# Performance work log

Hardware: AMD Instinct MI355X
Metric: run time of the kernel (lower is better)

## Reference

```python
import jax, jax.numpy as jnp
import numpy as np

B, N, M, C, H, D = 1, 4096, 4096, 768, 12, 64  # batch, tgt len, src len, in_dim, heads, head_dim
SCALE = D ** -0.5


def setup_inputs() -> dict:
    key = jax.random.key(0)
    ks = jax.random.split(key, 6)
    s = 0.02
    return {
        "x": jax.random.normal(ks[0], (B, N, C), jnp.float32),
        "src": jax.random.normal(ks[1], (B, M, C), jnp.float32),
        "W_qv": jax.random.normal(ks[2], (2 * H * D, C), jnp.float32) * s,
        "W_k": jax.random.normal(ks[3], (H * D, C), jnp.float32) * s,
        "W_proj": jax.random.normal(ks[4], (C, H * D), jnp.float32) * s,
        "b_proj": jnp.zeros((C,), jnp.float32),
    }


def reference(x, src, W_qv, W_k, W_proj, b_proj):
    Bb, Nn, _ = x.shape
    Mm = src.shape[1]
    # q, v come from src; k comes from x (info flows src -> target)
    qv = (src @ W_qv.T).reshape(Bb, Mm, 2, H, D)
    q = qv[:, :, 0].transpose(0, 2, 1, 3)  # (B, H, M, D)
    v = qv[:, :, 1].transpose(0, 2, 1, 3)  # (B, H, M, D)
    k = (x @ W_k.T).reshape(Bb, Nn, H, D) * SCALE  # (B, N, H, D), pre-scaled
    # attn[b,h,n,m] = q[b,h,m,:] . k[b,n,h,:]  (torch: (q @ k).transpose(-2,-1))
    attn = jnp.einsum('bhmd,bnhd->bhnm', q, k)
    attn = jax.nn.softmax(attn, axis=-1)  # softmax over src tokens m
    y = jnp.einsum('bhnm,bhmd->bnhd', attn, v).reshape(Bb, Nn, H * D)
    return y @ W_proj.T + b_proj
```

## Files before the change

### kernel.cpp

```cpp
#include <hip/hip_runtime.h>

using f32x4 = __attribute__((ext_vector_type(4))) float;
using s16x8 = __attribute__((ext_vector_type(8))) short;
using u16x4 = __attribute__((ext_vector_type(4))) unsigned short;

#define AS1 __attribute__((address_space(1)))
#define AS3 __attribute__((address_space(3)))

__device__ __forceinline__ void gload16(const void* g, void* l) {
  __builtin_amdgcn_global_load_lds((const AS1 unsigned int*)g,
                                   (AS3 unsigned int*)l, 16, 0, 0);
}

__device__ __forceinline__ unsigned short f2bf(float f) {
  unsigned int u = __builtin_bit_cast(unsigned int, f);
  u += 0x7fffu + ((u >> 16) & 1u);
  return (unsigned short)(u >> 16);
}

__device__ __forceinline__ unsigned int cvtpk(float lo, float hi) {
  unsigned int w;
  asm("v_cvt_pk_bf16_f32 %0, %1, %2" : "=v"(w) : "v"(lo), "v"(hi));
  return w;
}

__global__ __launch_bounds__(256) void cvt_bf16_multi(
    const float* __restrict__ i0, const float* __restrict__ i1,
    const float* __restrict__ i2, const float* __restrict__ i3,
    const float* __restrict__ i4, unsigned short* __restrict__ o0,
    unsigned short* __restrict__ o1, unsigned short* __restrict__ o2,
    unsigned short* __restrict__ o3, unsigned short* __restrict__ o4) {
  int b = blockIdx.x;
  const float* in;
  unsigned short* out;
  int base, n4;
  if (b < 3072) { in = i0; out = o0; base = b; n4 = 786432; }
  else if (b < 6144) { in = i1; out = o1; base = b - 3072; n4 = 786432; }
  else if (b < 7296) { in = i2; out = o2; base = b - 6144; n4 = 294912; }
  else if (b < 7872) { in = i3; out = o3; base = b - 7296; n4 = 147456; }
  else { in = i4; out = o4; base = b - 7872; n4 = 147456; }
  int i = base * 256 + threadIdx.x;
  if (i >= n4) return;
  f32x4 v = ((const f32x4*)in)[i];
  u16x4 r;
#pragma unroll
  for (int j = 0; j < 4; ++j) r[j] = f2bf(v[j]);
  ((u16x4*)out)[i] = r;
}

__global__ __launch_bounds__(256) void gemm_proj(
    const unsigned short* __restrict__ srcb, const unsigned short* __restrict__ wqvb,
    const unsigned short* __restrict__ xb, const unsigned short* __restrict__ wkb,
    unsigned short* __restrict__ qbuf, unsigned short* __restrict__ vtbuf,
    unsigned short* __restrict__ kbuf) {
  __shared__ __align__(16) unsigned short As[128 * 64];
  __shared__ __align__(16) unsigned short Bs[128 * 64];
  const bool isqv = blockIdx.y < 12;
  const unsigned short* A = isqv ? srcb : xb;
  const unsigned short* B = isqv ? wqvb : wkb;
  const int n0 = (isqv ? blockIdx.y : (blockIdx.y - 12)) * 128;
  const int m0 = blockIdx.x * 128;
  const int t = threadIdx.x;
  const int lane = t & 63;
  const int wid = t >> 6;
  const int wr = wid >> 1, wc = wid & 1;
  const int fr = lane & 15, fq = lane >> 4;

  f32x4 acc[4][4];
#pragma unroll
  for (int i = 0; i < 4; ++i)
#pragma unroll
    for (int j = 0; j < 4; ++j) acc[i][j] = (f32x4){0.f, 0.f, 0.f, 0.f};

  const char* Ab = (const char*)A;
  const char* Bb = (const char*)B;

  for (int k0 = 0; k0 < 768; k0 += 64) {
#pragma unroll
    for (int p = 0; p < 4; ++p) {
      int idx = p * 256 + t;
      int row = idx >> 3;
      int scb = ((idx & 7) << 4) ^ ((row & 7) << 4);
      char* dstA = (char*)As + (p * 256 + (wid << 6)) * 16;
      char* dstB = (char*)Bs + (p * 256 + (wid << 6)) * 16;
      gload16(Ab + (size_t)(m0 + row) * 1536 + (size_t)k0 * 2 + scb, dstA);
      gload16(Bb + (size_t)(n0 + row) * 1536 + (size_t)k0 * 2 + scb, dstB);
    }
    __syncthreads();

    s16x8 af[4][2], bfr[4][2];
#pragma unroll
    for (int mi = 0; mi < 4; ++mi)
#pragma unroll
      for (int kk = 0; kk < 2; ++kk) {
        int row = wr * 64 + mi * 16 + fr;
        int cb = (kk * 64 + (fq << 4)) ^ ((row & 7) << 4);
        af[mi][kk] = *(const s16x8*)((const char*)As + row * 128 + cb);
      }
#pragma unroll
    for (int ni = 0; ni < 4; ++ni)
#pragma unroll
      for (int kk = 0; kk < 2; ++kk) {
        int row = wc * 64 + ni * 16 + fr;
        int cb = (kk * 64 + (fq << 4)) ^ ((row & 7) << 4);
        bfr[ni][kk] = *(const s16x8*)((const char*)Bs + row * 128 + cb);
      }
    __builtin_amdgcn_s_setprio(1);
#pragma unroll
    for (int kk = 0; kk < 2; ++kk)
#pragma unroll
      for (int mi = 0; mi < 4; ++mi)
#pragma unroll
        for (int ni = 0; ni < 4; ++ni)
          acc[mi][ni] = __builtin_amdgcn_mfma_f32_16x16x32_bf16(
              af[mi][kk], bfr[ni][kk], acc[mi][ni], 0, 0, 0);
    __builtin_amdgcn_s_setprio(0);
    __syncthreads();
  }

#pragma unroll
  for (int mi = 0; mi < 4; ++mi) {
#pragma unroll
    for (int ni = 0; ni < 4; ++ni) {
      int row0 = m0 + wr * 64 + mi * 16 + (fq << 2);
      int col = n0 + wc * 64 + ni * 16 + fr;
      if (isqv) {
        if (n0 < 768) {
#pragma unroll
          for (int j = 0; j < 4; ++j)
            qbuf[(size_t)(row0 + j) * 768 + col] = f2bf(acc[mi][ni][j]);
        } else {
          u16x4 pk;
#pragma unroll
          for (int j = 0; j < 4; ++j) pk[j] = f2bf(acc[mi][ni][j]);
          *(u16x4*)(vtbuf + (size_t)(col - 768) * 4096 + row0) = pk;
        }
      } else {
#pragma unroll
        for (int j = 0; j < 4; ++j)
          kbuf[(size_t)(row0 + j) * 768 + col] = f2bf(acc[mi][ni][j] * 0.18033688f);
      }
    }
  }
}

__global__ __launch_bounds__(256) void gemm_out(
    const unsigned short* __restrict__ A, const unsigned short* __restrict__ B,
    float* __restrict__ outp, const float* __restrict__ bias) {
  __shared__ __align__(16) unsigned short As[128 * 64];
  __shared__ __align__(16) unsigned short Bs[128 * 64];
  const int t = threadIdx.x;
  const int lane = t & 63;
  const int wid = t >> 6;
  const int wr = wid >> 1, wc = wid & 1;
  const int m0 = blockIdx.x * 128, n0 = blockIdx.y * 128;
  const int fr = lane & 15, fq = lane >> 4;

  f32x4 acc[4][4];
#pragma unroll
  for (int i = 0; i < 4; ++i)
#pragma unroll
    for (int j = 0; j < 4; ++j) acc[i][j] = (f32x4){0.f, 0.f, 0.f, 0.f};

  for (int k0 = 0; k0 < 768; k0 += 64) {
#pragma unroll
    for (int p = 0; p < 4; ++p) {
      int idx = p * 256 + t;
      int row = idx >> 3;
      int scb = ((idx & 7) << 4) ^ ((row & 7) << 4);
      char* dstA = (char*)As + (p * 256 + (wid << 6)) * 16;
      char* dstB = (char*)Bs + (p * 256 + (wid << 6)) * 16;
      gload16((const char*)A + (size_t)(m0 + row) * 1536 + (size_t)k0 * 2 + scb, dstA);
      gload16((const char*)B + (size_t)(n0 + row) * 1536 + (size_t)k0 * 2 + scb, dstB);
    }
    __syncthreads();

    s16x8 af[4][2], bfr[4][2];
#pragma unroll
    for (int mi = 0; mi < 4; ++mi)
#pragma unroll
      for (int kk = 0; kk < 2; ++kk) {
        int row = wr * 64 + mi * 16 + fr;
        int cb = (kk * 64 + (fq << 4)) ^ ((row & 7) << 4);
        af[mi][kk] = *(const s16x8*)((const char*)As + row * 128 + cb);
      }
#pragma unroll
    for (int ni = 0; ni < 4; ++ni)
#pragma unroll
      for (int kk = 0; kk < 2; ++kk) {
        int row = wc * 64 + ni * 16 + fr;
        int cb = (kk * 64 + (fq << 4)) ^ ((row & 7) << 4);
        bfr[ni][kk] = *(const s16x8*)((const char*)Bs + row * 128 + cb);
      }
    __builtin_amdgcn_s_setprio(1);
#pragma unroll
    for (int kk = 0; kk < 2; ++kk)
#pragma unroll
      for (int mi = 0; mi < 4; ++mi)
#pragma unroll
        for (int ni = 0; ni < 4; ++ni)
          acc[mi][ni] = __builtin_amdgcn_mfma_f32_16x16x32_bf16(
              af[mi][kk], bfr[ni][kk], acc[mi][ni], 0, 0, 0);
    __builtin_amdgcn_s_setprio(0);
    __syncthreads();
  }

#pragma unroll
  for (int mi = 0; mi < 4; ++mi) {
#pragma unroll
    for (int ni = 0; ni < 4; ++ni) {
      int row0 = m0 + wr * 64 + mi * 16 + (fq << 2);
      int col = n0 + wc * 64 + ni * 16 + fr;
      float bv = bias[col];
#pragma unroll
      for (int j = 0; j < 4; ++j)
        outp[(size_t)(row0 + j) * 768 + col] = acc[mi][ni][j] + bv;
    }
  }
}

__global__ __launch_bounds__(256, 2) void attn_kernel(
    const unsigned short* __restrict__ Qk, const unsigned short* __restrict__ Kq,
    const unsigned short* __restrict__ Vt, unsigned short* __restrict__ Y) {
  __shared__ __align__(16) unsigned short Ks[2][64 * 64];
  __shared__ __align__(16) unsigned short Vs[2][64 * 64];
  __shared__ __align__(16) unsigned short Ps[4 * 16 * 64];
  const int t = threadIdx.x, lane = t & 63, wid = t >> 6;
  const int fr = lane & 15, fq = lane >> 4;

  int bid = blockIdx.x;
  int f = (bid & 7) * 96 + (bid >> 3);
  const int h = f >> 6;
  const int n0 = (f & 63) * 64;
  const int swz = (fr & 7) << 4;

  s16x8 qf[2];
  {
    const size_t qrow = n0 + wid * 16 + fr;
#pragma unroll
    for (int kk = 0; kk < 2; ++kk)
      qf[kk] = *(const s16x8*)(Qk + qrow * 768 + h * 64 + kk * 32 + fq * 8);
  }

  f32x4 o[4];
#pragma unroll
  for (int c = 0; c < 4; ++c) o[c] = (f32x4){0.f, 0.f, 0.f, 0.f};
  float lsum = 0.f;
  char* Pb = (char*)Ps + wid * 2048 + fr * 128;

  auto stage = [&](int buf, int m0) {
#pragma unroll
    for (int p = 0; p < 2; ++p) {
      int idx = p * 256 + t;
      int row = idx >> 3;
      int scb = ((idx & 7) << 4) ^ ((row & 7) << 4);
      char* dk = (char*)Ks[buf] + (p * 256 + (wid << 6)) * 16;
      char* dv = (char*)Vs[buf] + (p * 256 + (wid << 6)) * 16;
      gload16((const char*)Kq + (size_t)(m0 + row) * 1536 + h * 128 + scb, dk);
      gload16((const char*)Vt + (size_t)(h * 64 + row) * 8192 + (size_t)m0 * 2 + scb, dv);
    }
  };

  stage(0, 0);
  __syncthreads();

  for (int it = 0; it < 64; ++it) {
    const int buf = it & 1;
    if (it < 63) stage(buf ^ 1, (it + 1) * 64);

    f32x4 s[4];
#pragma unroll
    for (int c = 0; c < 4; ++c) s[c] = (f32x4){0.f, 0.f, 0.f, 0.f};
    const char* Ksb = (const char*)Ks[buf];
    const char* Vsb = (const char*)Vs[buf];
    __builtin_amdgcn_s_setprio(1);
#pragma unroll
    for (int kk = 0; kk < 2; ++kk)
#pragma unroll
      for (int c = 0; c < 4; ++c) {
        int row = c * 16 + fr;
        s16x8 kf = *(const s16x8*)(Ksb + row * 128 +
                                   ((kk * 64 + (fq << 4)) ^ ((row & 7) << 4)));
        s[c] = __builtin_amdgcn_mfma_f32_16x16x32_bf16(kf, qf[kk], s[c], 0, 0, 0);
      }
    __builtin_amdgcn_s_setprio(0);

#pragma unroll
    for (int c = 0; c < 4; ++c)
#pragma unroll
      for (int j = 0; j < 4; ++j) {
        s[c][j] = __builtin_exp2f(s[c][j]);
        lsum += s[c][j];
      }
#pragma unroll
    for (int c = 0; c < 4; ++c) {
      uint2 u;
      u.x = cvtpk(s[c][0], s[c][1]);
      u.y = cvtpk(s[c][2], s[c][3]);
      *(uint2*)(Pb + ((32 * c + 8 * fq) ^ swz)) = u;
    }

    __builtin_amdgcn_s_setprio(1);
#pragma unroll
    for (int kk = 0; kk < 2; ++kk) {
      s16x8 pa = *(const s16x8*)(Pb + ((kk * 64 + (fq << 4)) ^ swz));
#pragma unroll
      for (int c = 0; c < 4; ++c) {
        int vrow = c * 16 + fr;
        s16x8 vf = *(const s16x8*)(Vsb + vrow * 128 +
                                   ((kk * 64 + (fq << 4)) ^ ((vrow & 7) << 4)));
        o[c] = __builtin_amdgcn_mfma_f32_16x16x32_bf16(pa, vf, o[c], 0, 0, 0);
      }
    }
    __builtin_amdgcn_s_setprio(0);
    __syncthreads();
  }

  lsum += __shfl_xor(lsum, 16);
  lsum += __shfl_xor(lsum, 32);
  float inv = 1.0f / lsum;
  float invo[4];
#pragma unroll
  for (int j = 0; j < 4; ++j) invo[j] = __shfl(inv, 4 * fq + j);
#pragma unroll
  for (int c = 0; c < 4; ++c)
#pragma unroll
    for (int j = 0; j < 4; ++j) {
      size_t row = n0 + wid * 16 + (fq << 2) + j;
      int col = h * 64 + c * 16 + fr;
      Y[row * 768 + col] = f2bf(o[c][j] * invo[j]);
    }
}

extern "C" void kernel_launch(void* const* d_in, const int* in_sizes, int n_in,
                              void* d_out, int out_size, void* d_ws,
                              size_t ws_size, hipStream_t stream) {
  const float* x = (const float*)d_in[0];
  const float* src = (const float*)d_in[1];
  const float* Wqv = (const float*)d_in[2];
  const float* Wk = (const float*)d_in[3];
  const float* Wp = (const float*)d_in[4];
  const float* bp = (const float*)d_in[5];
  float* out = (float*)d_out;

  char* ws = (char*)d_ws;
  unsigned short* srcb = (unsigned short*)(ws + 0);
  unsigned short* xb   = (unsigned short*)(ws + 6291456);
  unsigned short* wqvb = (unsigned short*)(ws + 12582912);
  unsigned short* wkb  = (unsigned short*)(ws + 14942208);
  unsigned short* wpb  = (unsigned short*)(ws + 16121856);
  unsigned short* qbuf = (unsigned short*)(ws + 17301504);
  unsigned short* vtbuf= (unsigned short*)(ws + 23592960);
  unsigned short* kbuf = (unsigned short*)(ws + 29884416);
  unsigned short* ybuf = (unsigned short*)(ws + 36175872);

  cvt_bf16_multi<<<8448, 256, 0, stream>>>(src, x, Wqv, Wk, Wp, srcb, xb, wqvb,
                                           wkb, wpb);

  gemm_proj<<<dim3(32, 18), 256, 0, stream>>>(srcb, wqvb, xb, wkb, qbuf, vtbuf,
                                              kbuf);
  attn_kernel<<<768, 256, 0, stream>>>(kbuf, qbuf, vtbuf, ybuf);
  gemm_out<<<dim3(32, 6), 256, 0, stream>>>(ybuf, wpb, out, bp);
}
```

Measured before the change: 166.2 us.

## Split attention over source halves and reuse K/V fragments across two query tiles

Each attention block now covers 128 target rows and half of the source tokens. Each wave computes two 16-row query tiles against the same LDS K and V fragments, which halves LDS fragment reads per MFMA, and occupancy is raised to three blocks per SIMD. Unnormalized fp32 partial outputs and row sums go to workspace buffers that reuse dead regions. A new combine kernel adds the two halves, normalizes and converts to bf16. The trade-off is extra fp32 global traffic, one more launch, and higher register pressure.

After: 152.1 us. -8.5%, faster.

```diff
diff --git a/kernel.cpp b/kernel.cpp
--- a/kernel.cpp
+++ b/kernel.cpp
@@ -219,34 +219,43 @@
   }
 }
 
-__global__ __launch_bounds__(256, 2) void attn_kernel(
+__global__ __launch_bounds__(256, 3) void attn_kernel(
     const unsigned short* __restrict__ Qk, const unsigned short* __restrict__ Kq,
-    const unsigned short* __restrict__ Vt, unsigned short* __restrict__ Y) {
+    const unsigned short* __restrict__ Vt, float* __restrict__ Po0,
+    float* __restrict__ Po1, float* __restrict__ Pl) {
   __shared__ __align__(16) unsigned short Ks[2][64 * 64];
   __shared__ __align__(16) unsigned short Vs[2][64 * 64];
-  __shared__ __align__(16) unsigned short Ps[4 * 16 * 64];
+  __shared__ __align__(16) unsigned short Ps[4][2][16 * 64];
   const int t = threadIdx.x, lane = t & 63, wid = t >> 6;
   const int fr = lane & 15, fq = lane >> 4;
 
   int bid = blockIdx.x;
   int f = (bid & 7) * 96 + (bid >> 3);
   const int h = f >> 6;
-  const int n0 = (f & 63) * 64;
+  const int rem = f & 63;
+  const int n0 = (rem >> 1) * 128;
+  const int sp = rem & 1;
+  const int mbase = sp * 2048;
   const int swz = (fr & 7) << 4;
 
-  s16x8 qf[2];
-  {
-    const size_t qrow = n0 + wid * 16 + fr;
+  s16x8 qf[2][2];
+#pragma unroll
+  for (int st = 0; st < 2; ++st) {
+    const size_t qrow = n0 + wid * 32 + st * 16 + fr;
 #pragma unroll
     for (int kk = 0; kk < 2; ++kk)
-      qf[kk] = *(const s16x8*)(Qk + qrow * 768 + h * 64 + kk * 32 + fq * 8);
-  }
-
-  f32x4 o[4];
-#pragma unroll
-  for (int c = 0; c < 4; ++c) o[c] = (f32x4){0.f, 0.f, 0.f, 0.f};
-  float lsum = 0.f;
-  char* Pb = (char*)Ps + wid * 2048 + fr * 128;
+      qf[st][kk] = *(const s16x8*)(Qk + qrow * 768 + h * 64 + kk * 32 + fq * 8);
+  }
+
+  f32x4 o0[4], o1[4];
+#pragma unroll
+  for (int c = 0; c < 4; ++c) {
+    o0[c] = (f32x4){0.f, 0.f, 0.f, 0.f};
+    o1[c] = (f32x4){0.f, 0.f, 0.f, 0.f};
+  }
+  float lsum0 = 0.f, lsum1 = 0.f;
+  char* Pb0 = (char*)&Ps[wid][0][0] + fr * 128;
+  char* Pb1 = (char*)&Ps[wid][1][0] + fr * 128;
 
   auto stage = [&](int buf, int m0) {
 #pragma unroll
@@ -261,16 +270,19 @@
     }
   };
 
-  stage(0, 0);
+  stage(0, mbase);
   __syncthreads();
 
-  for (int it = 0; it < 64; ++it) {
+  for (int it = 0; it < 32; ++it) {
     const int buf = it & 1;
-    if (it < 63) stage(buf ^ 1, (it + 1) * 64);
-
-    f32x4 s[4];
-#pragma unroll
-    for (int c = 0; c < 4; ++c) s[c] = (f32x4){0.f, 0.f, 0.f, 0.f};
+    if (it < 31) stage(buf ^ 1, mbase + (it + 1) * 64);
+
+    f32x4 sA[4], sB[4];
+#pragma unroll
+    for (int c = 0; c < 4; ++c) {
+      sA[c] = (f32x4){0.f, 0.f, 0.f, 0.f};
+      sB[c] = (f32x4){0.f, 0.f, 0.f, 0.f};
+    }
     const char* Ksb = (const char*)Ks[buf];
     const char* Vsb = (const char*)Vs[buf];
     __builtin_amdgcn_s_setprio(1);
@@ -281,7 +293,8 @@
         int row = c * 16 + fr;
         s16x8 kf = *(const s16x8*)(Ksb + row * 128 +
                                    ((kk * 64 + (fq << 4)) ^ ((row & 7) << 4)));
-        s[c] = __builtin_amdgcn_mfma_f32_16x16x32_bf16(kf, qf[kk], s[c], 0, 0, 0);
+        sA[c] = __builtin_amdgcn_mfma_f32_16x16x32_bf16(kf, qf[0][kk], sA[c], 0, 0, 0);
+        sB[c] = __builtin_amdgcn_mfma_f32_16x16x32_bf16(kf, qf[1][kk], sB[c], 0, 0, 0);
       }
     __builtin_amdgcn_s_setprio(0);
 
@@ -289,47 +302,76 @@
     for (int c = 0; c < 4; ++c)
 #pragma unroll
       for (int j = 0; j < 4; ++j) {
-        s[c][j] = __builtin_exp2f(s[c][j]);
-        lsum += s[c][j];
+        sA[c][j] = __builtin_exp2f(sA[c][j]);
+        lsum0 += sA[c][j];
+        sB[c][j] = __builtin_exp2f(sB[c][j]);
+        lsum1 += sB[c][j];
       }
 #pragma unroll
     for (int c = 0; c < 4; ++c) {
-      uint2 u;
-      u.x = cvtpk(s[c][0], s[c][1]);
-      u.y = cvtpk(s[c][2], s[c][3]);
-      *(uint2*)(Pb + ((32 * c + 8 * fq) ^ swz)) = u;
+      uint2 ua, ub;
+      ua.x = cvtpk(sA[c][0], sA[c][1]);
+      ua.y = cvtpk(sA[c][2], sA[c][3]);
+      ub.x = cvtpk(sB[c][0], sB[c][1]);
+      ub.y = cvtpk(sB[c][2], sB[c][3]);
+      *(uint2*)(Pb0 + ((32 * c + 8 * fq) ^ swz)) = ua;
+      *(uint2*)(Pb1 + ((32 * c + 8 * fq) ^ swz)) = ub;
     }
 
     __builtin_amdgcn_s_setprio(1);
 #pragma unroll
     for (int kk = 0; kk < 2; ++kk) {
-      s16x8 pa = *(const s16x8*)(Pb + ((kk * 64 + (fq << 4)) ^ swz));
+      s16x8 pa0 = *(const s16x8*)(Pb0 + ((kk * 64 + (fq << 4)) ^ swz));
+      s16x8 pa1 = *(const s16x8*)(Pb1 + ((kk * 64 + (fq << 4)) ^ swz));
 #pragma unroll
       for (int c = 0; c < 4; ++c) {
         int vrow = c * 16 + fr;
         s16x8 vf = *(const s16x8*)(Vsb + vrow * 128 +
                                    ((kk * 64 + (fq << 4)) ^ ((vrow & 7) << 4)));
-        o[c] = __builtin_amdgcn_mfma_f32_16x16x32_bf16(pa, vf, o[c], 0, 0, 0);
+        o0[c] = __builtin_amdgcn_mfma_f32_16x16x32_bf16(pa0, vf, o0[c], 0, 0, 0);
+        o1[c] = __builtin_amdgcn_mfma_f32_16x16x32_bf16(pa1, vf, o1[c], 0, 0, 0);
       }
     }
     __builtin_amdgcn_s_setprio(0);
     __syncthreads();
   }
 
-  lsum += __shfl_xor(lsum, 16);
-  lsum += __shfl_xor(lsum, 32);
-  float inv = 1.0f / lsum;
-  float invo[4];
-#pragma unroll
-  for (int j = 0; j < 4; ++j) invo[j] = __shfl(inv, 4 * fq + j);
+  float* Po = sp ? Po1 : Po0;
+  lsum0 += __shfl_xor(lsum0, 16);
+  lsum0 += __shfl_xor(lsum0, 32);
+  lsum1 += __shfl_xor(lsum1, 16);
+  lsum1 += __shfl_xor(lsum1, 32);
+  if (fq == 0) {
+    Pl[sp * 49152 + (size_t)(n0 + wid * 32 + fr) * 12 + h] = lsum0;
+    Pl[sp * 49152 + (size_t)(n0 + wid * 32 + 16 + fr) * 12 + h] = lsum1;
+  }
 #pragma unroll
   for (int c = 0; c < 4; ++c)
 #pragma unroll
     for (int j = 0; j < 4; ++j) {
-      size_t row = n0 + wid * 16 + (fq << 2) + j;
+      size_t r0 = n0 + wid * 32 + (fq << 2) + j;
       int col = h * 64 + c * 16 + fr;
-      Y[row * 768 + col] = f2bf(o[c][j] * invo[j]);
-    }
+      Po[r0 * 768 + col] = o0[c][j];
+      Po[(r0 + 16) * 768 + col] = o1[c][j];
+    }
+}
+
+__global__ __launch_bounds__(256) void attn_combine(
+    const float* __restrict__ Po0, const float* __restrict__ Po1,
+    const float* __restrict__ Pl, unsigned short* __restrict__ Y) {
+  int idx = blockIdx.x * 256 + threadIdx.x;
+  int row = idx / 192;
+  int c4 = idx - row * 192;
+  int col = c4 * 4;
+  int h = col >> 6;
+  float l = Pl[(size_t)row * 12 + h] + Pl[49152 + (size_t)row * 12 + h];
+  float inv = 1.0f / l;
+  f32x4 a = *(const f32x4*)(Po0 + (size_t)row * 768 + col);
+  f32x4 b = *(const f32x4*)(Po1 + (size_t)row * 768 + col);
+  u16x4 r;
+#pragma unroll
+  for (int e = 0; e < 4; ++e) r[e] = f2bf((a[e] + b[e]) * inv);
+  *(u16x4*)(Y + (size_t)row * 768 + col) = r;
 }
 
 extern "C" void kernel_launch(void* const* d_in, const int* in_sizes, int n_in,
@@ -353,12 +395,16 @@
   unsigned short* vtbuf= (unsigned short*)(ws + 23592960);
   unsigned short* kbuf = (unsigned short*)(ws + 29884416);
   unsigned short* ybuf = (unsigned short*)(ws + 36175872);
+  float* part0 = (float*)(ws + 0);
+  float* lsums = (float*)(ws + 12582912);
+  float* part1 = (float*)(ws + 42467328);
 
   cvt_bf16_multi<<<8448, 256, 0, stream>>>(src, x, Wqv, Wk, Wp, srcb, xb, wqvb,
                                            wkb, wpb);
 
   gemm_proj<<<dim3(32, 18), 256, 0, stream>>>(srcb, wqvb, xb, wkb, qbuf, vtbuf,
                                               kbuf);
-  attn_kernel<<<768, 256, 0, stream>>>(kbuf, qbuf, vtbuf, ybuf);
+  attn_kernel<<<768, 256, 0, stream>>>(kbuf, qbuf, vtbuf, part0, part1, lsums);
+  attn_combine<<<3072, 256, 0, stream>>>(part0, part1, lsums, ybuf);
   gemm_out<<<dim3(32, 6), 256, 0, stream>>>(ybuf, wpb, out, bp);
 }
```
